# Kernel tuning notes

Measured on AMD Instinct MI355X. Metric: run time of the kernel, lower is better.

## Reference

```python
import jax, jax.numpy as jnp
import numpy as np

B, K, D = 2, 2048, 1024
H, DQ, DV = 16, 64, 64
DFF = 4096
ATT_SIZE = 256
LN_EPS = 1e-5


def _layernorm(x, g, b):
    mu = jnp.mean(x, axis=-1, keepdims=True)
    var = jnp.mean(jnp.square(x - mu), axis=-1, keepdims=True)
    return (x - mu) * jax.lax.rsqrt(var + LN_EPS) * g + b


def setup_inputs() -> dict:
    key = jax.random.key(0)
    ks = jax.random.split(key, 16)
    s = lambda d: 1.0 / np.sqrt(d)
    return {
        "x": jax.random.normal(ks[0], (B, K, D), dtype=jnp.float32),
        "Wq": jax.random.normal(ks[1], (D, H * DQ), dtype=jnp.float32) * s(D),
        "bq": jnp.zeros((H * DQ,), dtype=jnp.float32),
        "Wk": jax.random.normal(ks[2], (D, H * DQ), dtype=jnp.float32) * s(D),
        "bk": jnp.zeros((H * DQ,), dtype=jnp.float32),
        "Wv": jax.random.normal(ks[3], (D, H * DV), dtype=jnp.float32) * s(D),
        "bv": jnp.zeros((H * DV,), dtype=jnp.float32),
        "Wo": jax.random.normal(ks[4], (H * DV, D), dtype=jnp.float32) * s(H * DV),
        "bo": jnp.zeros((D,), dtype=jnp.float32),
        "W1": jax.random.normal(ks[5], (D, DFF), dtype=jnp.float32) * s(D),
        "b1": jnp.zeros((DFF,), dtype=jnp.float32),
        "W2": jax.random.normal(ks[6], (DFF, D), dtype=jnp.float32) * s(DFF),
        "b2": jnp.zeros((D,), dtype=jnp.float32),
        "ln1_g": jnp.ones((D,), dtype=jnp.float32),
        "ln1_b": jnp.zeros((D,), dtype=jnp.float32),
        "ln2_g": jnp.ones((D,), dtype=jnp.float32),
        "ln2_b": jnp.zeros((D,), dtype=jnp.float32),
    }


def reference(x, Wq, bq, Wk, bk, Wv, bv, Wo, bo, W1, b1, W2, b2,
              ln1_g, ln1_b, ln2_g, ln2_b):
    b, k, d = x.shape
    # --- multi-head attention (heads formed by chunking last dim) ---
    q = (x @ Wq + bq).reshape(b, k, H, DQ)  # [b,k,h,dq]
    kk = (x @ Wk + bk).reshape(b, k, H, DQ)
    v = (x @ Wv + bv).reshape(b, k, H, DV)
    # NOTE: original scales by sqrt(K) (sequence length), not sqrt(d_q)
    scores = jnp.einsum('bshd,bthd->bhst', q, kk) / jnp.sqrt(jnp.float32(k))
    idx = jnp.arange(k)
    band_mask = jnp.abs(idx[:, None] - idx[None, :]) > ATT_SIZE  # [k,k] bool
    scores = jnp.where(band_mask[None, None], -jnp.inf, scores)
    attn = jax.nn.softmax(scores, axis=-1)
    ctx = jnp.einsum('bhst,bthd->bshd', attn, v).reshape(b, k, H * DV)
    sa = ctx @ Wo + bo
    x1 = _layernorm(sa + x, ln1_g, ln1_b)
    # --- position-wise FFN (exact GELU as torch F.gelu default) ---
    ff = (jax.nn.gelu(x1 @ W1 + b1, approximate=False)) @ W2 + b2
    return _layernorm(ff + x1, ln2_g, ln2_b)
```

## Files before the change

### kernel.cpp

```cpp
#include <hip/hip_runtime.h>
#include <cstdint>
#include <math.h>

typedef unsigned short u16;
typedef __attribute__((ext_vector_type(8))) short bf16x8;
typedef __attribute__((ext_vector_type(4))) float f32x4;

#define DEVI __device__ __forceinline__

DEVI u16 f2bf(float f) {
  union { float f; uint32_t u; } v; v.f = f;
  return (u16)((v.u + 0x7FFFu + ((v.u >> 16) & 1u)) >> 16);
}
DEVI float bf2f(u16 h) {
  union { uint32_t u; float f; } v; v.u = ((uint32_t)h) << 16;
  return v.f;
}

DEVI void gload16(const void* g, void* l) {
  __builtin_amdgcn_global_load_lds(
      (const __attribute__((address_space(1))) void*)g,
      (__attribute__((address_space(3))) void*)l, 16, 0, 0);
}

DEVI float gelu_fast(float u) {
  float u2 = u * u;
  float t = __builtin_fmaf(0.044715f * u2, u, u);
  float e = __expf(1.5957691216057308f * t);
  float r = __builtin_amdgcn_rcpf(1.0f + e);
  return u - u * r;
}

DEVI void tcvt_body(const float* __restrict__ W, u16* __restrict__ Wt,
                    int Kd, int N, int n0, int k0, float* t) {
  const int r = threadIdx.x >> 4, c4 = (threadIdx.x & 15) * 4;
#pragma unroll
  for (int p = 0; p < 4; ++p) {
    int row = p * 16 + r;
    float4 f = *(const float4*)(W + (size_t)(k0 + row) * N + n0 + c4);
    *(float4*)&t[row * 68 + c4] = f;
  }
  __syncthreads();
#pragma unroll
  for (int p = 0; p < 4; ++p) {
    int n = p * 16 + r;
    float v0 = t[(c4 + 0) * 68 + n];
    float v1 = t[(c4 + 1) * 68 + n];
    float v2 = t[(c4 + 2) * 68 + n];
    float v3 = t[(c4 + 3) * 68 + n];
    uint32_t lo = (uint32_t)f2bf(v0) | ((uint32_t)f2bf(v1) << 16);
    uint32_t hi = (uint32_t)f2bf(v2) | ((uint32_t)f2bf(v3) << 16);
    *(uint2*)(Wt + (size_t)(n0 + n) * Kd + k0 + c4) = make_uint2(lo, hi);
  }
}

__global__ __launch_bounds__(256)
void prep_kernel(const float* __restrict__ Wq, const float* __restrict__ Wk,
                 const float* __restrict__ Wv, const float* __restrict__ Wo,
                 const float* __restrict__ W1, const float* __restrict__ W2,
                 const float* __restrict__ x, const float* __restrict__ bq,
                 const float* __restrict__ bk, const float* __restrict__ bv,
                 u16* __restrict__ WqkvT, u16* __restrict__ WoT,
                 u16* __restrict__ W1T, u16* __restrict__ W2T,
                 u16* __restrict__ xb, float* __restrict__ bqkv)
{
  __shared__ float t[64 * 68];
  const int b = blockIdx.x;
  if (b < 1024) {
    int wsel = b >> 8, tt = b & 255;
    const float* W = (wsel == 0) ? Wq : (wsel == 1) ? Wk : (wsel == 2) ? Wv : Wo;
    u16* dst = (wsel == 3) ? WoT : WqkvT + (size_t)wsel * 1024 * 1024;
    tcvt_body(W, dst, 1024, 1024, (tt & 15) * 64, (tt >> 4) * 64, t);
  } else if (b < 2048) {
    int tt = b - 1024;
    tcvt_body(W1, W1T, 1024, 4096, (tt & 63) * 64, (tt >> 6) * 64, t);
  } else if (b < 3072) {
    int tt = b - 2048;
    tcvt_body(W2, W2T, 4096, 1024, (tt & 15) * 64, (tt >> 4) * 64, t);
  } else if (b < 7168) {
    int i = ((b - 3072) * 256 + threadIdx.x) * 4;
    float4 f = *(const float4*)(x + i);
    uint32_t lo = (uint32_t)f2bf(f.x) | ((uint32_t)f2bf(f.y) << 16);
    uint32_t hi = (uint32_t)f2bf(f.z) | ((uint32_t)f2bf(f.w) << 16);
    *(uint2*)(xb + i) = make_uint2(lo, hi);
  } else {
    int i = (b - 7168) * 256 + threadIdx.x;
    const float* s = (i < 1024) ? bq : ((i < 2048) ? bk : bv);
    bqkv[i] = s[i & 1023];
  }
}

template<int MODE>
__global__ __launch_bounds__(256, 4)
void gemm_kernel(const u16* __restrict__ A, const u16* __restrict__ Bt,
                 const float* __restrict__ bias, void* __restrict__ C0,
                 void* __restrict__ C1, int N, int Kfull, int Kpart)
{
  __shared__ u16 As0[128 * 32], As1[128 * 32];
  __shared__ u16 Bs0[128 * 32], Bs1[128 * 32];
  const int tid = threadIdx.x;
  const int nbx = gridDim.x, nby = gridDim.y;
  int lin = blockIdx.y * nbx + blockIdx.x;
  int band = lin / (8 * nbx);
  int rem = lin - band * (8 * nbx);
  int gsz = min(nby - band * 8, 8);
  const int m0 = (band * 8 + rem % gsz) * 128;
  const int n0 = (rem / gsz) * 128;
  const int kbase = (MODE == 2) ? (int)blockIdx.z * Kpart : 0;
  const int w = tid >> 6, lane = tid & 63;
  const int wm = (w >> 1) * 64, wn = (w & 1) * 64;
  const int mr = lane & 15, ko = (lane >> 4) * 8;
  const int rq = (lane >> 4) * 4;
  const int w32 = w * 32;

  f32x4 acc[4][4];
#pragma unroll
  for (int i = 0; i < 4; ++i)
#pragma unroll
    for (int j = 0; j < 4; ++j) {
      f32x4 z = {0.f, 0.f, 0.f, 0.f};
      acc[i][j] = z;
    }

  const int lr = lane >> 2, lk = (lane & 3) * 8;
  const u16* aG = A  + (size_t)(m0 + w32 + lr) * Kfull + kbase + lk;
  const u16* bG = Bt + (size_t)(n0 + w32 + lr) * Kfull + kbase + lk;
  u16* aD00 = &As0[(w32 +  0) * 32];
  u16* aD01 = &As0[(w32 + 16) * 32];
  u16* aD10 = &As1[(w32 +  0) * 32];
  u16* aD11 = &As1[(w32 + 16) * 32];
  u16* bD00 = &Bs0[(w32 +  0) * 32];
  u16* bD01 = &Bs0[(w32 + 16) * 32];
  u16* bD10 = &Bs1[(w32 +  0) * 32];
  u16* bD11 = &Bs1[(w32 + 16) * 32];
  const size_t row16 = (size_t)16 * Kfull;

  for (int k0 = 0; k0 < Kpart; k0 += 64) {
    gload16(aG + k0,              aD00);
    gload16(aG + row16 + k0,      aD01);
    gload16(aG + k0 + 32,         aD10);
    gload16(aG + row16 + k0 + 32, aD11);
    gload16(bG + k0,              bD00);
    gload16(bG + row16 + k0,      bD01);
    gload16(bG + k0 + 32,         bD10);
    gload16(bG + row16 + k0 + 32, bD11);
    __syncthreads();
#pragma unroll
    for (int s = 0; s < 2; ++s) {
      const u16* Ap = s ? As1 : As0;
      const u16* Bp = s ? Bs1 : Bs0;
      bf16x8 af[4], bf[4];
#pragma unroll
      for (int i = 0; i < 4; ++i)
        af[i] = *(const bf16x8*)&Ap[(wm + i * 16 + mr) * 32 + ko];
#pragma unroll
      for (int j = 0; j < 4; ++j)
        bf[j] = *(const bf16x8*)&Bp[(wn + j * 16 + mr) * 32 + ko];
#pragma unroll
      for (int i = 0; i < 4; ++i)
#pragma unroll
        for (int j = 0; j < 4; ++j)
          acc[i][j] = __builtin_amdgcn_mfma_f32_16x16x32_bf16(bf[j], af[i], acc[i][j], 0, 0, 0);
    }
    __syncthreads();
  }

  if (MODE == 0) {
    if (n0 < 2048) {
#pragma unroll
      for (int i = 0; i < 4; ++i) {
        size_t mrow = (size_t)(m0 + wm + i * 16 + mr) * 2048;
#pragma unroll
        for (int j = 0; j < 4; ++j) {
          int nb = n0 + wn + j * 16 + rq;
          float4 b4 = *(const float4*)&bias[nb];
          uint32_t lo = (uint32_t)f2bf(acc[i][j][0] + b4.x) |
                        ((uint32_t)f2bf(acc[i][j][1] + b4.y) << 16);
          uint32_t hi = (uint32_t)f2bf(acc[i][j][2] + b4.z) |
                        ((uint32_t)f2bf(acc[i][j][3] + b4.w) << 16);
          *(uint2*)((u16*)C0 + mrow + nb) = make_uint2(lo, hi);
        }
      }
    } else {
#pragma unroll
      for (int i = 0; i < 4; ++i) {
        int mg = m0 + wm + i * 16 + mr;
#pragma unroll
        for (int j = 0; j < 4; ++j) {
          int nb = n0 + wn + j * 16 + rq;
          float4 b4 = *(const float4*)&bias[nb];
          int d = nb - 2048;
          ((u16*)C1)[(size_t)(d + 0) * 4096 + mg] = f2bf(acc[i][j][0] + b4.x);
          ((u16*)C1)[(size_t)(d + 1) * 4096 + mg] = f2bf(acc[i][j][1] + b4.y);
          ((u16*)C1)[(size_t)(d + 2) * 4096 + mg] = f2bf(acc[i][j][2] + b4.z);
          ((u16*)C1)[(size_t)(d + 3) * 4096 + mg] = f2bf(acc[i][j][3] + b4.w);
        }
      }
    }
  } else {
    const bool part1 = (MODE == 2) && (blockIdx.z == 1);
#pragma unroll
    for (int i = 0; i < 4; ++i) {
      size_t mrow = (size_t)(m0 + wm + i * 16 + mr) * N;
#pragma unroll
      for (int j = 0; j < 4; ++j) {
        int nb = n0 + wn + j * 16 + rq;
        float v0 = acc[i][j][0], v1 = acc[i][j][1];
        float v2 = acc[i][j][2], v3 = acc[i][j][3];
        if (!part1) {
          float4 b4 = *(const float4*)&bias[nb];
          v0 += b4.x; v1 += b4.y; v2 += b4.z; v3 += b4.w;
        }
        if (MODE == 1) {
          v0 = gelu_fast(v0); v1 = gelu_fast(v1);
          v2 = gelu_fast(v2); v3 = gelu_fast(v3);
        }
        uint32_t lo = (uint32_t)f2bf(v0) | ((uint32_t)f2bf(v1) << 16);
        uint32_t hi = (uint32_t)f2bf(v2) | ((uint32_t)f2bf(v3) << 16);
        u16* dst = part1 ? (u16*)C1 : (u16*)C0;
        *(uint2*)(dst + mrow + nb) = make_uint2(lo, hi);
      }
    }
  }
}

__global__ __launch_bounds__(256)
void attn_kernel(const u16* __restrict__ QKb, const u16* __restrict__ Vt,
                 u16* __restrict__ ctx)
{
  const int KS = 2048, HD = 1024;
  __shared__ u16 Qs[64 * 80];
  __shared__ u16 Ks[64 * 80];
  __shared__ u16 Vts[64 * 72];
  __shared__ u16 Ps[64 * 72];

  const int qt = blockIdx.x, hh = blockIdx.y, bb = blockIdx.z;
  const int s0 = qt * 64;
  const int tid = threadIdx.x, w = tid >> 6, lane = tid & 63;
  const int mr = lane & 15, ko = (lane >> 4) * 8, rq = (lane >> 4) * 4;
  const int sr = tid >> 3, sc = (tid & 7) * 8;
  const int vrow = tid >> 2, vtc = (tid & 3) * 16;
  const float qsc = 0.022097086912079608f;
  const int qg = s0 + w * 16 + mr;

#pragma unroll
  for (int p = 0; p < 2; ++p) {
    int row = p * 32 + sr;
    uint4 u = *(const uint4*)(QKb + (size_t)(bb * KS + s0 + row) * 2048 + hh * 64 + sc);
    *(uint4*)&Qs[row * 80 + sc] = u;
  }

  f32x4 accO[4];
#pragma unroll
  for (int j = 0; j < 4; ++j) { f32x4 z = {0.f,0.f,0.f,0.f}; accO[j] = z; }
  float lsum = 0.f;

  for (int c = 0; c < 9; ++c) {
    int tb = s0 - 256 + c * 64;
    if (tb < 0 || tb >= KS) continue;
    __syncthreads();
#pragma unroll
    for (int p = 0; p < 2; ++p) {
      int row = p * 32 + sr;
      uint4 uk = *(const uint4*)(QKb + (size_t)(bb * KS + tb + row) * 2048 + 1024 + hh * 64 + sc);
      *(uint4*)&Ks[row * 80 + sc] = uk;
    }
    {
      const u16* vsrc = Vt + (size_t)(hh * 64 + vrow) * 4096 + bb * KS + tb + vtc;
      *(uint4*)&Vts[vrow * 72 + vtc]     = *(const uint4*)vsrc;
      *(uint4*)&Vts[vrow * 72 + vtc + 8] = *(const uint4*)(vsrc + 8);
    }
    __syncthreads();

    f32x4 sacc[4];
#pragma unroll
    for (int j = 0; j < 4; ++j) { f32x4 z = {0.f,0.f,0.f,0.f}; sacc[j] = z; }
#pragma unroll
    for (int s = 0; s < 2; ++s) {
      bf16x8 aq = *(const bf16x8*)&Qs[(w * 16 + mr) * 80 + s * 32 + ko];
#pragma unroll
      for (int j = 0; j < 4; ++j) {
        bf16x8 bk = *(const bf16x8*)&Ks[(j * 16 + mr) * 80 + s * 32 + ko];
        sacc[j] = __builtin_amdgcn_mfma_f32_16x16x32_bf16(bk, aq, sacc[j], 0, 0, 0);
      }
    }

#pragma unroll
    for (int j = 0; j < 4; ++j) {
      int tgb = tb + j * 16 + rq;
      float p0, p1, p2, p3;
      {
        int d0 = qg - tgb;
        float s_ = sacc[j][0] * qsc;
        p0 = (d0 > 256 || d0 < -256) ? 0.f : __expf(s_);
        int d1 = d0 - 1; s_ = sacc[j][1] * qsc;
        p1 = (d1 > 256 || d1 < -256) ? 0.f : __expf(s_);
        int d2 = d0 - 2; s_ = sacc[j][2] * qsc;
        p2 = (d2 > 256 || d2 < -256) ? 0.f : __expf(s_);
        int d3 = d0 - 3; s_ = sacc[j][3] * qsc;
        p3 = (d3 > 256 || d3 < -256) ? 0.f : __expf(s_);
      }
      lsum += p0 + p1 + p2 + p3;
      uint32_t lo = (uint32_t)f2bf(p0) | ((uint32_t)f2bf(p1) << 16);
      uint32_t hi = (uint32_t)f2bf(p2) | ((uint32_t)f2bf(p3) << 16);
      *(uint2*)&Ps[(w * 16 + mr) * 72 + j * 16 + rq] = make_uint2(lo, hi);
    }
#pragma unroll
    for (int s = 0; s < 2; ++s) {
      bf16x8 ap = *(const bf16x8*)&Ps[(w * 16 + mr) * 72 + s * 32 + ko];
#pragma unroll
      for (int j = 0; j < 4; ++j) {
        bf16x8 bv = *(const bf16x8*)&Vts[(j * 16 + mr) * 72 + s * 32 + ko];
        accO[j] = __builtin_amdgcn_mfma_f32_16x16x32_bf16(bv, ap, accO[j], 0, 0, 0);
      }
    }
  }

  float l = lsum;
  l += __shfl_xor(l, 16, 64);
  l += __shfl_xor(l, 32, 64);
  float inv = 1.f / l;
  size_t base = (size_t)(bb * KS + qg) * HD + hh * 64;
#pragma unroll
  for (int j = 0; j < 4; ++j) {
    uint32_t lo = (uint32_t)f2bf(accO[j][0] * inv) | ((uint32_t)f2bf(accO[j][1] * inv) << 16);
    uint32_t hi = (uint32_t)f2bf(accO[j][2] * inv) | ((uint32_t)f2bf(accO[j][3] * inv) << 16);
    *(uint2*)(ctx + base + j * 16 + rq) = make_uint2(lo, hi);
  }
}

DEVI void bfadd4(const u16* p, size_t base, float& v0, float& v1, float& v2, float& v3) {
  uint2 u = *(const uint2*)(p + base);
  v0 += bf2f((u16)(u.x & 0xFFFFu));
  v1 += bf2f((u16)(u.x >> 16));
  v2 += bf2f((u16)(u.y & 0xFFFFu));
  v3 += bf2f((u16)(u.y >> 16));
}

template<int OUT32>
__global__ __launch_bounds__(256)
void ln_kernel(const u16* __restrict__ p0, const u16* __restrict__ p1,
               const u16* __restrict__ res, const float* __restrict__ g,
               const float* __restrict__ be, void* __restrict__ out)
{
  __shared__ float red[8];
  const int row = blockIdx.x, tid = threadIdx.x;
  const int w = tid >> 6, lane = tid & 63;
  size_t base = (size_t)row * 1024 + tid * 4;
  float v0 = 0.f, v1 = 0.f, v2 = 0.f, v3 = 0.f;
  bfadd4(p0, base, v0, v1, v2, v3);
  bfadd4(p1, base, v0, v1, v2, v3);
  bfadd4(res, base, v0, v1, v2, v3);
  float s1 = v0 + v1 + v2 + v3;
  float s2 = v0 * v0 + v1 * v1 + v2 * v2 + v3 * v3;
#pragma unroll
  for (int o = 32; o > 0; o >>= 1) {
    s1 += __shfl_xor(s1, o, 64);
    s2 += __shfl_xor(s2, o, 64);
  }
  if (lane == 0) { red[w] = s1; red[4 + w] = s2; }
  __syncthreads();
  s1 = red[0] + red[1] + red[2] + red[3];
  s2 = red[4] + red[5] + red[6] + red[7];
  float mu = s1 * (1.f / 1024.f);
  float var = s2 * (1.f / 1024.f) - mu * mu;
  float rs = rsqrtf(var + 1e-5f);
  float4 gv = *(const float4*)(g + tid * 4);
  float4 bv = *(const float4*)(be + tid * 4);
  float o0 = (v0 - mu) * rs * gv.x + bv.x;
  float o1 = (v1 - mu) * rs * gv.y + bv.y;
  float o2 = (v2 - mu) * rs * gv.z + bv.z;
  float o3 = (v3 - mu) * rs * gv.w + bv.w;
  if (OUT32) {
    float4 ov; ov.x = o0; ov.y = o1; ov.z = o2; ov.w = o3;
    *(float4*)((float*)out + base) = ov;
  } else {
    uint32_t lo = (uint32_t)f2bf(o0) | ((uint32_t)f2bf(o1) << 16);
    uint32_t hi = (uint32_t)f2bf(o2) | ((uint32_t)f2bf(o3) << 16);
    *(uint2*)((u16*)out + base) = make_uint2(lo, hi);
  }
}

extern "C" void kernel_launch(void* const* d_in, const int* in_sizes, int n_in,
                              void* d_out, int out_size, void* d_ws, size_t ws_size,
                              hipStream_t stream)
{
  (void)in_sizes; (void)n_in; (void)out_size; (void)ws_size;
  const float* x   = (const float*)d_in[0];
  const float* Wq  = (const float*)d_in[1];
  const float* bq  = (const float*)d_in[2];
  const float* Wk  = (const float*)d_in[3];
  const float* bk  = (const float*)d_in[4];
  const float* Wv  = (const float*)d_in[5];
  const float* bv  = (const float*)d_in[6];
  const float* Wo  = (const float*)d_in[7];
  const float* bo  = (const float*)d_in[8];
  const float* W1  = (const float*)d_in[9];
  const float* b1  = (const float*)d_in[10];
  const float* W2  = (const float*)d_in[11];
  const float* b2  = (const float*)d_in[12];
  const float* g1  = (const float*)d_in[13];
  const float* be1 = (const float*)d_in[14];
  const float* g2  = (const float*)d_in[15];
  const float* be2 = (const float*)d_in[16];

  char* ws = (char*)d_ws;
  const size_t MB = 1048576;
  u16*   W1T   = (u16*)(ws + 0 * MB);
  u16*   Y0b   = (u16*)(ws + 0 * MB);
  u16*   xb    = (u16*)(ws + 8 * MB);
  u16*   Y1b   = (u16*)(ws + 8 * MB);
  u16*   WqkvT = (u16*)(ws + 16 * MB);
  u16*   X1b   = (u16*)(ws + 16 * MB);
  u16*   WoT   = (u16*)(ws + 22 * MB);
  u16*   QKb   = (u16*)(ws + 24 * MB);
  u16*   SA0b  = (u16*)(ws + 24 * MB);
  u16*   SA1b  = (u16*)(ws + 32 * MB);
  u16*   Hb    = (u16*)(ws + 24 * MB);
  u16*   Vt    = (u16*)(ws + 40 * MB);
  float* bqkv  = (float*)(ws + 48 * MB);
  u16*   Cb    = (u16*)(ws + 48 * MB);
  u16*   W2T   = (u16*)(ws + 56 * MB);
  float* yout  = (float*)d_out;

  dim3 blk(256);
  prep_kernel<<<7180, blk, 0, stream>>>(Wq, Wk, Wv, Wo, W1, W2, x, bq, bk, bv,
                                        WqkvT, WoT, W1T, W2T, xb, bqkv);
  gemm_kernel<0><<<dim3(24, 32, 1), blk, 0, stream>>>(xb, WqkvT, bqkv, QKb, Vt, 3072, 1024, 1024);
  attn_kernel<<<dim3(32, 16, 2), blk, 0, stream>>>(QKb, Vt, Cb);
  gemm_kernel<2><<<dim3(8, 32, 2), blk, 0, stream>>>(Cb, WoT, bo, SA0b, SA1b, 1024, 1024, 512);
  ln_kernel<0><<<4096, blk, 0, stream>>>(SA0b, SA1b, xb, g1, be1, X1b);
  gemm_kernel<1><<<dim3(32, 32, 1), blk, 0, stream>>>(X1b, W1T, b1, Hb, nullptr, 4096, 1024, 1024);
  gemm_kernel<2><<<dim3(8, 32, 2), blk, 0, stream>>>(Hb, W2T, b2, Y0b, Y1b, 1024, 4096, 2048);
  ln_kernel<1><<<4096, blk, 0, stream>>>(Y0b, Y1b, X1b, g2, be2, yout);
}
```

Before: 313.0 us.

## Add 256x256-tile 8-wave GEMM kernel for QKV and FFN1 projections

```diff
diff --git a/kernel.cpp b/kernel.cpp
--- a/kernel.cpp
+++ b/kernel.cpp
@@ -165,39 +165,7 @@
     __syncthreads();
   }
 
-  if (MODE == 0) {
-    if (n0 < 2048) {
-#pragma unroll
-      for (int i = 0; i < 4; ++i) {
-        size_t mrow = (size_t)(m0 + wm + i * 16 + mr) * 2048;
-#pragma unroll
-        for (int j = 0; j < 4; ++j) {
-          int nb = n0 + wn + j * 16 + rq;
-          float4 b4 = *(const float4*)&bias[nb];
-          uint32_t lo = (uint32_t)f2bf(acc[i][j][0] + b4.x) |
-                        ((uint32_t)f2bf(acc[i][j][1] + b4.y) << 16);
-          uint32_t hi = (uint32_t)f2bf(acc[i][j][2] + b4.z) |
-                        ((uint32_t)f2bf(acc[i][j][3] + b4.w) << 16);
-          *(uint2*)((u16*)C0 + mrow + nb) = make_uint2(lo, hi);
-        }
-      }
-    } else {
-#pragma unroll
-      for (int i = 0; i < 4; ++i) {
-        int mg = m0 + wm + i * 16 + mr;
-#pragma unroll
-        for (int j = 0; j < 4; ++j) {
-          int nb = n0 + wn + j * 16 + rq;
-          float4 b4 = *(const float4*)&bias[nb];
-          int d = nb - 2048;
-          ((u16*)C1)[(size_t)(d + 0) * 4096 + mg] = f2bf(acc[i][j][0] + b4.x);
-          ((u16*)C1)[(size_t)(d + 1) * 4096 + mg] = f2bf(acc[i][j][1] + b4.y);
-          ((u16*)C1)[(size_t)(d + 2) * 4096 + mg] = f2bf(acc[i][j][2] + b4.z);
-          ((u16*)C1)[(size_t)(d + 3) * 4096 + mg] = f2bf(acc[i][j][3] + b4.w);
-        }
-      }
-    }
-  } else {
+  {
     const bool part1 = (MODE == 2) && (blockIdx.z == 1);
 #pragma unroll
     for (int i = 0; i < 4; ++i) {
@@ -219,6 +187,169 @@
         uint32_t hi = (uint32_t)f2bf(v2) | ((uint32_t)f2bf(v3) << 16);
         u16* dst = part1 ? (u16*)C1 : (u16*)C0;
         *(uint2*)(dst + mrow + nb) = make_uint2(lo, hi);
+      }
+    }
+  }
+}
+
+#define VMW4 asm volatile("s_waitcnt vmcnt(4)" ::: "memory")
+#define VMW2 asm volatile("s_waitcnt vmcnt(2)" ::: "memory")
+#define VMW0 asm volatile("s_waitcnt vmcnt(0)" ::: "memory")
+#define VMWN
+
+DEVI void stage_half(const u16* __restrict__ G, int row0, int Kfull, int tk,
+                     u16* lds_half, int w, int srow, int scol) {
+  const u16* s = G + (size_t)(row0 + w * 8 + srow) * Kfull + tk + scol;
+  u16* d = lds_half + w * 512;
+  gload16(s, d);
+  gload16(s + ((size_t)Kfull << 6), d + 4096);
+}
+
+#define PH(MH, NH, WAIT) do {                                                 \
+    const u16* Ab_ = &As[(cur * 2 + (MH)) * 8192];                            \
+    const u16* Bb_ = &Bs[(cur * 2 + (NH)) * 8192];                            \
+    bf16x8 a0_[4], a1_[4], b0_[2], b1_[2];                                    \
+    _Pragma("unroll")                                                         \
+    for (int i_ = 0; i_ < 4; ++i_) {                                          \
+      const u16* p_ = Ab_ + (wm * 64 + i_ * 16 + mr) * 64;                    \
+      a0_[i_] = *(const bf16x8*)(p_ + c0);                                    \
+      a1_[i_] = *(const bf16x8*)(p_ + c1);                                    \
+    }                                                                         \
+    _Pragma("unroll")                                                         \
+    for (int j_ = 0; j_ < 2; ++j_) {                                          \
+      const u16* p_ = Bb_ + (wn * 32 + j_ * 16 + mr) * 64;                    \
+      b0_[j_] = *(const bf16x8*)(p_ + c0);                                    \
+      b1_[j_] = *(const bf16x8*)(p_ + c1);                                    \
+    }                                                                         \
+    __builtin_amdgcn_s_barrier();                                             \
+    __builtin_amdgcn_s_setprio(1);                                            \
+    _Pragma("unroll")                                                         \
+    for (int i_ = 0; i_ < 4; ++i_)                                            \
+      _Pragma("unroll")                                                       \
+      for (int j_ = 0; j_ < 2; ++j_) {                                        \
+        acc[(MH)*4+i_][(NH)*2+j_] = __builtin_amdgcn_mfma_f32_16x16x32_bf16(  \
+            b0_[j_], a0_[i_], acc[(MH)*4+i_][(NH)*2+j_], 0, 0, 0);            \
+        acc[(MH)*4+i_][(NH)*2+j_] = __builtin_amdgcn_mfma_f32_16x16x32_bf16(  \
+            b1_[j_], a1_[i_], acc[(MH)*4+i_][(NH)*2+j_], 0, 0, 0);            \
+      }                                                                       \
+    __builtin_amdgcn_s_setprio(0);                                            \
+    WAIT;                                                                     \
+    __builtin_amdgcn_s_barrier();                                             \
+  } while (0)
+
+template<int MODE>
+__global__ __launch_bounds__(512, 2)
+void gemm256_kernel(const u16* __restrict__ A, const u16* __restrict__ Bt,
+                    const float* __restrict__ bias, void* __restrict__ C0,
+                    void* __restrict__ C1, int N, int Kfull, int NBN)
+{
+  __shared__ u16 As[32768];
+  __shared__ u16 Bs[32768];
+  const int tid = threadIdx.x;
+  const int w = tid >> 6, lane = tid & 63;
+  const int wm = w >> 2, wn = w & 3;
+  const int mr = lane & 15;
+  const int rq = (lane >> 4) * 4;
+
+  const int lin = blockIdx.x;
+  const int q = gridDim.x >> 3;
+  const int wg = (lin & 7) * q + (lin >> 3);
+  const int mt = wg / NBN, nt = wg - mt * NBN;
+  const int m0 = mt * 256, n0 = nt * 256;
+
+  const int srow = lane >> 3;
+  const int scol = ((lane & 7) ^ srow) << 3;
+  const int bl = (lane >> 4) << 4;
+  const int sw = (mr & 7) << 4;
+  const int c0 = (bl ^ sw) >> 1;
+  const int c1 = ((64 + bl) ^ sw) >> 1;
+
+  f32x4 acc[8][4];
+#pragma unroll
+  for (int i = 0; i < 8; ++i)
+#pragma unroll
+    for (int j = 0; j < 4; ++j) {
+      f32x4 z = {0.f, 0.f, 0.f, 0.f};
+      acc[i][j] = z;
+    }
+
+  const int NT = Kfull >> 6;
+
+  stage_half(A,  m0 + 0,   Kfull, 0, &As[0],    w, srow, scol);
+  stage_half(Bt, n0 + 0,   Kfull, 0, &Bs[0],    w, srow, scol);
+  stage_half(Bt, n0 + 128, Kfull, 0, &Bs[8192], w, srow, scol);
+  stage_half(A,  m0 + 128, Kfull, 0, &As[8192], w, srow, scol);
+  VMW4;
+  __builtin_amdgcn_s_barrier();
+
+  int t = 0;
+  for (; t < NT - 1; ++t) {
+    const int cur = t & 1, nxt = cur ^ 1, k1 = (t + 1) * 64;
+    stage_half(A,  m0 + 0,   Kfull, k1, &As[(nxt*2+0)*8192], w, srow, scol);
+    PH(0, 0, VMW4);
+    stage_half(Bt, n0 + 0,   Kfull, k1, &Bs[(nxt*2+0)*8192], w, srow, scol);
+    PH(0, 1, VMW4);
+    stage_half(Bt, n0 + 128, Kfull, k1, &Bs[(nxt*2+1)*8192], w, srow, scol);
+    PH(1, 1, VMW4);
+    stage_half(A,  m0 + 128, Kfull, k1, &As[(nxt*2+1)*8192], w, srow, scol);
+    PH(1, 0, VMW4);
+  }
+  {
+    const int cur = t & 1;
+    PH(0, 0, VMW2);
+    PH(0, 1, VMW0);
+    PH(1, 1, VMWN);
+    PH(1, 0, VMWN);
+  }
+
+  if (MODE == 0) {
+    if (n0 < 2048) {
+#pragma unroll
+      for (int mi = 0; mi < 8; ++mi) {
+        int mg = m0 + (mi >> 2) * 128 + wm * 64 + (mi & 3) * 16 + mr;
+        size_t mrow = (size_t)mg * 2048;
+#pragma unroll
+        for (int ni = 0; ni < 4; ++ni) {
+          int ng = n0 + (ni >> 1) * 128 + wn * 32 + (ni & 1) * 16 + rq;
+          float4 b4 = *(const float4*)&bias[ng];
+          f32x4 a = acc[mi][ni];
+          uint32_t lo = (uint32_t)f2bf(a[0] + b4.x) | ((uint32_t)f2bf(a[1] + b4.y) << 16);
+          uint32_t hi = (uint32_t)f2bf(a[2] + b4.z) | ((uint32_t)f2bf(a[3] + b4.w) << 16);
+          *(uint2*)((u16*)C0 + mrow + ng) = make_uint2(lo, hi);
+        }
+      }
+    } else {
+#pragma unroll
+      for (int mi = 0; mi < 8; ++mi) {
+        int mg = m0 + (mi >> 2) * 128 + wm * 64 + (mi & 3) * 16 + mr;
+#pragma unroll
+        for (int ni = 0; ni < 4; ++ni) {
+          int ng = n0 + (ni >> 1) * 128 + wn * 32 + (ni & 1) * 16 + rq;
+          float4 b4 = *(const float4*)&bias[ng];
+          f32x4 a = acc[mi][ni];
+          int d = ng - 2048;
+          ((u16*)C1)[(size_t)(d + 0) * 4096 + mg] = f2bf(a[0] + b4.x);
+          ((u16*)C1)[(size_t)(d + 1) * 4096 + mg] = f2bf(a[1] + b4.y);
+          ((u16*)C1)[(size_t)(d + 2) * 4096 + mg] = f2bf(a[2] + b4.z);
+          ((u16*)C1)[(size_t)(d + 3) * 4096 + mg] = f2bf(a[3] + b4.w);
+        }
+      }
+    }
+  } else {
+#pragma unroll
+    for (int mi = 0; mi < 8; ++mi) {
+      int mg = m0 + (mi >> 2) * 128 + wm * 64 + (mi & 3) * 16 + mr;
+      size_t mrow = (size_t)mg * N;
+#pragma unroll
+      for (int ni = 0; ni < 4; ++ni) {
+        int ng = n0 + (ni >> 1) * 128 + wn * 32 + (ni & 1) * 16 + rq;
+        float4 b4 = *(const float4*)&bias[ng];
+        f32x4 a = acc[mi][ni];
+        float v0 = gelu_fast(a[0] + b4.x), v1 = gelu_fast(a[1] + b4.y);
+        float v2 = gelu_fast(a[2] + b4.z), v3 = gelu_fast(a[3] + b4.w);
+        uint32_t lo = (uint32_t)f2bf(v0) | ((uint32_t)f2bf(v1) << 16);
+        uint32_t hi = (uint32_t)f2bf(v2) | ((uint32_t)f2bf(v3) << 16);
+        *(uint2*)((u16*)C0 + mrow + ng) = make_uint2(lo, hi);
       }
     }
   }
@@ -424,13 +555,14 @@
   float* yout  = (float*)d_out;
 
   dim3 blk(256);
+  dim3 blk512(512);
   prep_kernel<<<7180, blk, 0, stream>>>(Wq, Wk, Wv, Wo, W1, W2, x, bq, bk, bv,
                                         WqkvT, WoT, W1T, W2T, xb, bqkv);
-  gemm_kernel<0><<<dim3(24, 32, 1), blk, 0, stream>>>(xb, WqkvT, bqkv, QKb, Vt, 3072, 1024, 1024);
+  gemm256_kernel<0><<<dim3(192), blk512, 0, stream>>>(xb, WqkvT, bqkv, QKb, Vt, 3072, 1024, 12);
   attn_kernel<<<dim3(32, 16, 2), blk, 0, stream>>>(QKb, Vt, Cb);
   gemm_kernel<2><<<dim3(8, 32, 2), blk, 0, stream>>>(Cb, WoT, bo, SA0b, SA1b, 1024, 1024, 512);
   ln_kernel<0><<<4096, blk, 0, stream>>>(SA0b, SA1b, xb, g1, be1, X1b);
-  gemm_kernel<1><<<dim3(32, 32, 1), blk, 0, stream>>>(X1b, W1T, b1, Hb, nullptr, 4096, 1024, 1024);
+  gemm256_kernel<1><<<dim3(256), blk512, 0, stream>>>(X1b, W1T, b1, Hb, nullptr, 4096, 1024, 16);
   gemm_kernel<2><<<dim3(8, 32, 2), blk, 0, stream>>>(Hb, W2T, b2, Y0b, Y1b, 1024, 4096, 2048);
   ln_kernel<1><<<4096, blk, 0, stream>>>(Y0b, Y1b, X1b, g2, be2, yout);
 }
```

Measured after the change: 339.5 us. 8.5% more time.

## Process two query tiles per attention block to reuse K/V tiles

Applied to the files above, without the earlier changes.

```diff
diff --git a/kernel.cpp b/kernel.cpp
--- a/kernel.cpp
+++ b/kernel.cpp
@@ -224,38 +224,81 @@
   }
 }
 
+#define QSET(AQ, QG, LSUM, ACCO) do {                                         \
+    f32x4 sacc[4];                                                            \
+    _Pragma("unroll")                                                         \
+    for (int j = 0; j < 4; ++j) { f32x4 z = {0.f,0.f,0.f,0.f}; sacc[j] = z; } \
+    _Pragma("unroll")                                                         \
+    for (int s = 0; s < 2; ++s) {                                             \
+      _Pragma("unroll")                                                       \
+      for (int j = 0; j < 4; ++j) {                                           \
+        bf16x8 bk = *(const bf16x8*)&Ks[(j * 16 + mr) * 80 + s * 32 + ko];    \
+        sacc[j] = __builtin_amdgcn_mfma_f32_16x16x32_bf16(bk, AQ[s], sacc[j], 0, 0, 0); \
+      }                                                                       \
+    }                                                                         \
+    _Pragma("unroll")                                                         \
+    for (int j = 0; j < 4; ++j) {                                             \
+      int tgb = tb + j * 16 + rq;                                             \
+      int d0 = (QG) - tgb;                                                    \
+      float s_ = sacc[j][0] * qsc;                                            \
+      float p0 = (d0 > 256 || d0 < -256) ? 0.f : __expf(s_);                  \
+      int d1 = d0 - 1; s_ = sacc[j][1] * qsc;                                 \
+      float p1 = (d1 > 256 || d1 < -256) ? 0.f : __expf(s_);                  \
+      int d2 = d0 - 2; s_ = sacc[j][2] * qsc;                                 \
+      float p2 = (d2 > 256 || d2 < -256) ? 0.f : __expf(s_);                  \
+      int d3 = d0 - 3; s_ = sacc[j][3] * qsc;                                 \
+      float p3 = (d3 > 256 || d3 < -256) ? 0.f : __expf(s_);                  \
+      LSUM += p0 + p1 + p2 + p3;                                              \
+      uint32_t lo = (uint32_t)f2bf(p0) | ((uint32_t)f2bf(p1) << 16);          \
+      uint32_t hi = (uint32_t)f2bf(p2) | ((uint32_t)f2bf(p3) << 16);          \
+      *(uint2*)&Ps[(w * 16 + mr) * 72 + j * 16 + rq] = make_uint2(lo, hi);    \
+    }                                                                         \
+    _Pragma("unroll")                                                         \
+    for (int s = 0; s < 2; ++s) {                                             \
+      bf16x8 ap = *(const bf16x8*)&Ps[(w * 16 + mr) * 72 + s * 32 + ko];      \
+      _Pragma("unroll")                                                       \
+      for (int j = 0; j < 4; ++j) {                                           \
+        bf16x8 bv = *(const bf16x8*)&Vts[(j * 16 + mr) * 72 + s * 32 + ko];   \
+        ACCO[j] = __builtin_amdgcn_mfma_f32_16x16x32_bf16(bv, ap, ACCO[j], 0, 0, 0); \
+      }                                                                       \
+    }                                                                         \
+  } while (0)
+
 __global__ __launch_bounds__(256)
 void attn_kernel(const u16* __restrict__ QKb, const u16* __restrict__ Vt,
                  u16* __restrict__ ctx)
 {
   const int KS = 2048, HD = 1024;
-  __shared__ u16 Qs[64 * 80];
   __shared__ u16 Ks[64 * 80];
   __shared__ u16 Vts[64 * 72];
   __shared__ u16 Ps[64 * 72];
 
   const int qt = blockIdx.x, hh = blockIdx.y, bb = blockIdx.z;
-  const int s0 = qt * 64;
+  const int s0 = qt * 128;
   const int tid = threadIdx.x, w = tid >> 6, lane = tid & 63;
   const int mr = lane & 15, ko = (lane >> 4) * 8, rq = (lane >> 4) * 4;
   const int sr = tid >> 3, sc = (tid & 7) * 8;
   const int vrow = tid >> 2, vtc = (tid & 3) * 16;
   const float qsc = 0.022097086912079608f;
-  const int qg = s0 + w * 16 + mr;
-
-#pragma unroll
-  for (int p = 0; p < 2; ++p) {
-    int row = p * 32 + sr;
-    uint4 u = *(const uint4*)(QKb + (size_t)(bb * KS + s0 + row) * 2048 + hh * 64 + sc);
-    *(uint4*)&Qs[row * 80 + sc] = u;
-  }
-
-  f32x4 accO[4];
-#pragma unroll
-  for (int j = 0; j < 4; ++j) { f32x4 z = {0.f,0.f,0.f,0.f}; accO[j] = z; }
-  float lsum = 0.f;
-
-  for (int c = 0; c < 9; ++c) {
+  const int qgA = s0 + w * 16 + mr;
+  const int qgB = qgA + 64;
+
+  bf16x8 aqA[2], aqB[2];
+#pragma unroll
+  for (int s = 0; s < 2; ++s) {
+    aqA[s] = *(const bf16x8*)(QKb + (size_t)(bb * KS + qgA) * 2048 + hh * 64 + s * 32 + ko);
+    aqB[s] = *(const bf16x8*)(QKb + (size_t)(bb * KS + qgB) * 2048 + hh * 64 + s * 32 + ko);
+  }
+
+  f32x4 accOA[4], accOB[4];
+#pragma unroll
+  for (int j = 0; j < 4; ++j) {
+    f32x4 z = {0.f,0.f,0.f,0.f};
+    accOA[j] = z; accOB[j] = z;
+  }
+  float lsumA = 0.f, lsumB = 0.f;
+
+  for (int c = 0; c < 10; ++c) {
     int tb = s0 - 256 + c * 64;
     if (tb < 0 || tb >= KS) continue;
     __syncthreads();
@@ -272,60 +315,28 @@
     }
     __syncthreads();
 
-    f32x4 sacc[4];
-#pragma unroll
-    for (int j = 0; j < 4; ++j) { f32x4 z = {0.f,0.f,0.f,0.f}; sacc[j] = z; }
-#pragma unroll
-    for (int s = 0; s < 2; ++s) {
-      bf16x8 aq = *(const bf16x8*)&Qs[(w * 16 + mr) * 80 + s * 32 + ko];
-#pragma unroll
-      for (int j = 0; j < 4; ++j) {
-        bf16x8 bk = *(const bf16x8*)&Ks[(j * 16 + mr) * 80 + s * 32 + ko];
-        sacc[j] = __builtin_amdgcn_mfma_f32_16x16x32_bf16(bk, aq, sacc[j], 0, 0, 0);
-      }
-    }
-
-#pragma unroll
-    for (int j = 0; j < 4; ++j) {
-      int tgb = tb + j * 16 + rq;
-      float p0, p1, p2, p3;
-      {
-        int d0 = qg - tgb;
-        float s_ = sacc[j][0] * qsc;
-        p0 = (d0 > 256 || d0 < -256) ? 0.f : __expf(s_);
-        int d1 = d0 - 1; s_ = sacc[j][1] * qsc;
-        p1 = (d1 > 256 || d1 < -256) ? 0.f : __expf(s_);
-        int d2 = d0 - 2; s_ = sacc[j][2] * qsc;
-        p2 = (d2 > 256 || d2 < -256) ? 0.f : __expf(s_);
-        int d3 = d0 - 3; s_ = sacc[j][3] * qsc;
-        p3 = (d3 > 256 || d3 < -256) ? 0.f : __expf(s_);
-      }
-      lsum += p0 + p1 + p2 + p3;
-      uint32_t lo = (uint32_t)f2bf(p0) | ((uint32_t)f2bf(p1) << 16);
-      uint32_t hi = (uint32_t)f2bf(p2) | ((uint32_t)f2bf(p3) << 16);
-      *(uint2*)&Ps[(w * 16 + mr) * 72 + j * 16 + rq] = make_uint2(lo, hi);
-    }
-#pragma unroll
-    for (int s = 0; s < 2; ++s) {
-      bf16x8 ap = *(const bf16x8*)&Ps[(w * 16 + mr) * 72 + s * 32 + ko];
-#pragma unroll
-      for (int j = 0; j < 4; ++j) {
-        bf16x8 bv = *(const bf16x8*)&Vts[(j * 16 + mr) * 72 + s * 32 + ko];
-        accO[j] = __builtin_amdgcn_mfma_f32_16x16x32_bf16(bv, ap, accO[j], 0, 0, 0);
-      }
-    }
-  }
-
-  float l = lsum;
-  l += __shfl_xor(l, 16, 64);
-  l += __shfl_xor(l, 32, 64);
-  float inv = 1.f / l;
-  size_t base = (size_t)(bb * KS + qg) * HD + hh * 64;
+    QSET(aqA, qgA, lsumA, accOA);
+    QSET(aqB, qgB, lsumB, accOB);
+  }
+
+  float lA = lsumA;
+  lA += __shfl_xor(lA, 16, 64);
+  lA += __shfl_xor(lA, 32, 64);
+  float invA = 1.f / lA;
+  float lB = lsumB;
+  lB += __shfl_xor(lB, 16, 64);
+  lB += __shfl_xor(lB, 32, 64);
+  float invB = 1.f / lB;
+  size_t baseA = (size_t)(bb * KS + qgA) * HD + hh * 64;
+  size_t baseB = (size_t)(bb * KS + qgB) * HD + hh * 64;
 #pragma unroll
   for (int j = 0; j < 4; ++j) {
-    uint32_t lo = (uint32_t)f2bf(accO[j][0] * inv) | ((uint32_t)f2bf(accO[j][1] * inv) << 16);
-    uint32_t hi = (uint32_t)f2bf(accO[j][2] * inv) | ((uint32_t)f2bf(accO[j][3] * inv) << 16);
-    *(uint2*)(ctx + base + j * 16 + rq) = make_uint2(lo, hi);
+    uint32_t loA = (uint32_t)f2bf(accOA[j][0] * invA) | ((uint32_t)f2bf(accOA[j][1] * invA) << 16);
+    uint32_t hiA = (uint32_t)f2bf(accOA[j][2] * invA) | ((uint32_t)f2bf(accOA[j][3] * invA) << 16);
+    *(uint2*)(ctx + baseA + j * 16 + rq) = make_uint2(loA, hiA);
+    uint32_t loB = (uint32_t)f2bf(accOB[j][0] * invB) | ((uint32_t)f2bf(accOB[j][1] * invB) << 16);
+    uint32_t hiB = (uint32_t)f2bf(accOB[j][2] * invB) | ((uint32_t)f2bf(accOB[j][3] * invB) << 16);
+    *(uint2*)(ctx + baseB + j * 16 + rq) = make_uint2(loB, hiB);
   }
 }
 
@@ -427,7 +438,7 @@
   prep_kernel<<<7180, blk, 0, stream>>>(Wq, Wk, Wv, Wo, W1, W2, x, bq, bk, bv,
                                         WqkvT, WoT, W1T, W2T, xb, bqkv);
   gemm_kernel<0><<<dim3(24, 32, 1), blk, 0, stream>>>(xb, WqkvT, bqkv, QKb, Vt, 3072, 1024, 1024);
-  attn_kernel<<<dim3(32, 16, 2), blk, 0, stream>>>(QKb, Vt, Cb);
+  attn_kernel<<<dim3(16, 16, 2), blk, 0, stream>>>(QKb, Vt, Cb);
   gemm_kernel<2><<<dim3(8, 32, 2), blk, 0, stream>>>(Cb, WoT, bo, SA0b, SA1b, 1024, 1024, 512);
   ln_kernel<0><<<4096, blk, 0, stream>>>(SA0b, SA1b, xb, g1, be1, X1b);
   gemm_kernel<1><<<dim3(32, 32, 1), blk, 0, stream>>>(X1b, W1T, b1, Hb, nullptr, 4096, 1024, 1024);
```

Result: slower. 325.7 us (+4.1%).
